# Kernel tuning notes

Measured on AMD Instinct MI355X. Metric: run time of the kernel, lower is better.

Reference implementation:

```python
import jax, jax.numpy as jnp
import numpy as np

# dims
B, T, N, E, ENC, HID, HEADS, D = 64, 128, 2000, 300, 256, 256, 5, 16
IN = ENC + 2 * E          # GRUCell input: assign_emb + program_emb + node_emb
ATT = HID * HEADS         # self-attention context dim (Lin et al. 2017 multi-head)


def setup_inputs() -> dict:
    key = jax.random.key(0)
    ks = jax.random.split(key, 16)
    f = lambda k, shp, s=0.05: jax.random.normal(k, shp, dtype=jnp.float32) * s
    return {
        "program_emb": f(ks[0], (B, ENC), 1.0),
        "h0": f(ks[1], (B, HID), 1.0),                 # xavier-like init h0
        "node_emb": f(ks[2], (N + 1, E)),              # nn.Embedding(num_nodes+1, E)
        "label_emb": f(ks[3], (N + 1, D, E)),          # per-node label embedding experts
        "gru_w_ih": f(ks[4], (3 * HID, IN)),
        "gru_w_hh": f(ks[5], (3 * HID, HID)),
        "gru_b_ih": f(ks[6], (3 * HID,)),
        "gru_b_hh": f(ks[7], (3 * HID,)),
        "attn_ws1": f(ks[8], (HID, HID)),              # SelfAttention ws1 (no bias)
        "attn_ws2": f(ks[9], (HEADS, HID)),            # SelfAttention ws2 (no bias)
        "pred_w": f(ks[10], (N + 1, ATT, D)),          # per-node Linear experts
        "pred_b": f(ks[11], (N + 1, D)),
        "execution_trace": jax.random.randint(ks[12], (B, T), 0, N + 1),
        "node_assignments": jax.random.randint(ks[13], (B, N), 0, D),
        "execution_lengths": jax.random.randint(ks[14], (B,), 1, T + 1),
    }


def _forward(program_emb, h0, node_emb, label_emb, gru_w_ih, gru_w_hh,
             gru_b_ih, gru_b_hh, attn_ws1, attn_ws2, pred_w, pred_b,
             execution_trace, node_assignments):
    # pad assignments with a zero column (PAD node indexes column N)
    na = jnp.concatenate(
        [node_assignments, jnp.zeros((B, 1), node_assignments.dtype)], axis=1)
    rows = jnp.arange(B)
    pos = jnp.arange(T - 1)

    def step(carry, xs):
        h, store = carry
        node_i, node_ip1, i = xs
        # routed label-embedding lookup: expert chosen by node id, row by assignment
        assign_emb = label_emb[node_i, na[rows, node_i]]        # [B,E]
        x = jnp.concatenate([assign_emb, program_emb, node_emb[node_i]], axis=1)
        # torch nn.GRUCell math
        gi = x @ gru_w_ih.T + gru_b_ih
        gh = h @ gru_w_hh.T + gru_b_hh
        ir, iz, inn = jnp.split(gi, 3, axis=1)
        hr, hz, hn = jnp.split(gh, 3, axis=1)
        r = jax.nn.sigmoid(ir + hr)
        z = jax.nn.sigmoid(iz + hz)
        n = jnp.tanh(inn + r * hn)
        h = (1.0 - z) * n + z * h
        # append to growing hidden_store (fixed buffer, step-i slot)
        store = jax.lax.dynamic_update_slice_in_dim(store, h[:, None, :], i, axis=1)
        # structured self-attention over all stored hiddens.
        # NOTE: attn_lengths = max(exec_len, len(store)) >= len(store), so the
        # length mask never hides any stored position; only unwritten slots mask.
        scores = jnp.tanh(store @ attn_ws1.T) @ attn_ws2.T      # [B,T-1,HEADS]
        scores = jnp.where((pos <= i)[None, :, None], scores, -1e9)
        alpha = jax.nn.softmax(scores, axis=1)                  # softmax over time
        ctx = jnp.einsum('bth,btd->bhd', alpha, store).reshape(B, ATT)
        # routed prediction head: expert chosen by next node id (grouped GEMM)
        out = jnp.einsum('bd,bdk->bk', ctx, pred_w[node_ip1]) + pred_b[node_ip1]
        return (h, store), (out, alpha)

    store0 = jnp.zeros((B, T - 1, HID), h0.dtype)
    xs = (execution_trace[:, :-1].T, execution_trace[:, 1:].T, jnp.arange(T - 1))
    (_, _), (outs, alphas) = jax.lax.scan(step, (h0, store0), xs)
    return outs, alphas  # [T-1,B,D], [T-1,B,T-1,HEADS]


def reference(program_emb, h0, node_emb, label_emb, gru_w_ih, gru_w_hh,
              gru_b_ih, gru_b_hh, attn_ws1, attn_ws2, pred_w, pred_b,
              execution_trace, node_assignments, execution_lengths):
    # execution_lengths only enters via max(exec_len, step+1) which never masks;
    # kept for interface fidelity.
    del execution_lengths
    return _forward(program_emb, h0, node_emb, label_emb, gru_w_ih, gru_w_hh,
                    gru_b_ih, gru_b_hh, attn_ws1, attn_ws2, pred_w, pred_b,
                    execution_trace, node_assignments)
```

## Files before the change

kernel.cpp:

```cpp
#include <hip/hip_runtime.h>
#include <hip/hip_bf16.h>
#include <math.h>

#define BB 64
#define TT 128
#define T1 127
#define NNODE 2000
#define EE 300
#define HID 256
#define NHEADS 5
#define DD 16
#define G3 768
#define ATT 1280
#define SCALE_H 28.0f

typedef _Float16 h2_t __attribute__((ext_vector_type(2)));
typedef short short8 __attribute__((ext_vector_type(8)));
typedef float f32x4 __attribute__((ext_vector_type(4)));

__device__ __forceinline__ int dot4(int a, int b, int c) {
#if __has_builtin(__builtin_amdgcn_sdot4)
    return __builtin_amdgcn_sdot4(a, b, c, false);
#else
    int r;
    asm("v_dot4_i32_i8 %0, %1, %2, %3" : "=v"(r) : "v"(a), "v"(b), "v"(c));
    return r;
#endif
}

__device__ __forceinline__ unsigned short f2bf(float f) {
    unsigned u = __float_as_uint(f);
    unsigned r = (u + 0x7FFFu + ((u >> 16) & 1u)) >> 16;
    return (unsigned short)r;
}

__global__ void k_tcvt2(const float* __restrict__ a, unsigned short* __restrict__ da, int Ra, int Ca,
                        const float* __restrict__ b, unsigned short* __restrict__ db, int Rb, int Cb) {
    int idx = blockIdx.x * 256 + threadIdx.x;
    int na = Ra * Ca;
    if (idx < na) {
        int r = idx / Ca, c = idx % Ca;
        da[c * Ra + r] = f2bf(a[idx]);
    } else {
        idx -= na;
        if (idx < Rb * Cb) {
            int r = idx / Cb, c = idx % Cb;
            db[c * Rb + r] = f2bf(b[idx]);
        }
    }
}

__global__ __launch_bounds__(64) void k_quant(const float* __restrict__ w, int* __restrict__ wq,
                                              float* __restrict__ wsc) {
    int row = blockIdx.x;
    int t = threadIdx.x;
    const float* wr = w + (size_t)row * HID;
    float4 v = *(const float4*)(wr + t * 4);
    float m = fmaxf(fmaxf(fabsf(v.x), fabsf(v.y)), fmaxf(fabsf(v.z), fabsf(v.w)));
#pragma unroll
    for (int off = 1; off < 64; off <<= 1) m = fmaxf(m, __shfl_xor(m, off));
    float s = (m > 0.f) ? m * (1.0f / 127.0f) : 1.0f;
    float inv = 1.0f / s;
    int q0 = max(-127, min(127, __float2int_rn(v.x * inv)));
    int q1 = max(-127, min(127, __float2int_rn(v.y * inv)));
    int q2 = max(-127, min(127, __float2int_rn(v.z * inv)));
    int q3 = max(-127, min(127, __float2int_rn(v.w * inv)));
    wq[row * 64 + t] = (q0 & 0xFF) | ((q1 & 0xFF) << 8) | ((q2 & 0xFF) << 16) | ((q3 & 0xFF) << 24);
    if (t == 0) wsc[row] = s;
}

__global__ __launch_bounds__(256) void k_mgemm(
    const float* __restrict__ A, const unsigned short* __restrict__ B16,
    float* __restrict__ out, const float* __restrict__ bias,
    const int* __restrict__ trace, const int* __restrict__ na,
    int mode, int M, int K, int N, int strideA, int ntiles, int brow0, int Bld, int dotanh)
{
    __shared__ short As[64][40];
    __shared__ short Bt[64][40];
    __shared__ int baseLds[64];
    __shared__ int validLds[64];
    int tid = threadIdx.x;
    int bm = blockIdx.x / ntiles, bn = blockIdx.x % ntiles;
    int m0 = bm * 64, n0 = bn * 64;
    if (tid < 64) {
        int m = m0 + tid;
        int valid = (m < M) ? 1 : 0;
        int base = 0;
        if (valid) {
            if (mode == 2) {
                int i = m >> 6, bb = m & 63;
                int node = trace[bb * TT + i];
                int asg = (node < NNODE) ? na[bb * NNODE + node] : 0;
                base = (node * DD + asg) * EE;
            } else {
                base = m * strideA;
            }
        }
        baseLds[tid] = base;
        validLds[tid] = valid;
    }
    __syncthreads();

    int wv = tid >> 6, l = tid & 63;
    int lr = l & 15, lg = l >> 4;
    f32x4 acc[4];
#pragma unroll
    for (int cb = 0; cb < 4; cb++) acc[cb] = (f32x4){0.f, 0.f, 0.f, 0.f};

    int ar = tid >> 2, aq = tid & 3;
    int bk = tid >> 3, bq = tid & 7;
    int nsteps = (K + 31) >> 5;
    for (int it = 0; it < nsteps; it++) {
        int kk = it * 32;
        {
            int base = baseLds[ar], val = validLds[ar];
            short8 t1;
#pragma unroll
            for (int j = 0; j < 8; j++) {
                int kx = kk + aq * 8 + j;
                float v = (val && kx < K) ? A[(size_t)base + kx] : 0.f;
                t1[j] = (short)f2bf(v);
            }
            *(short8*)&As[ar][aq * 8] = t1;
        }
        {
            int kx = kk + bk;
            short8 t2;
            if (kx < K) {
                t2 = *(const short8*)(B16 + (size_t)(brow0 + kx) * Bld + n0 + bq * 8);
            } else {
#pragma unroll
                for (int j = 0; j < 8; j++) t2[j] = 0;
            }
#pragma unroll
            for (int j = 0; j < 8; j++) Bt[bq * 8 + j][bk] = t2[j];
        }
        __syncthreads();
        short8 a = *(const short8*)&As[wv * 16 + lr][lg * 8];
#pragma unroll
        for (int cb = 0; cb < 4; cb++) {
            short8 bfr = *(const short8*)&Bt[cb * 16 + lr][lg * 8];
            acc[cb] = __builtin_amdgcn_mfma_f32_16x16x32_bf16(a, bfr, acc[cb], 0, 0, 0);
        }
        __syncthreads();
    }
#pragma unroll
    for (int cb = 0; cb < 4; cb++) {
        int col = n0 + cb * 16 + lr;
#pragma unroll
        for (int q = 0; q < 4; q++) {
            int row = m0 + wv * 16 + lg * 4 + q;
            if (row < M) {
                float v = acc[cb][q];
                if (bias) v += bias[col];
                if (dotanh) v = tanhf(v);
                out[(size_t)row * N + col] = v;
            }
        }
    }
}

#define LG_PITCH 328
__global__ __launch_bounds__(256) void k_lgemm2(
    const float* __restrict__ A, const unsigned short* __restrict__ B16,
    const float* __restrict__ node_t, const float* __restrict__ prog_t,
    const int* __restrict__ trace, const int* __restrict__ na,
    float* __restrict__ out)
{
    __shared__ short Afull[64][LG_PITCH];
    __shared__ short Bt[64][40];
    __shared__ int nodeLds[64];
    const int tid = threadIdx.x;
    const int ib = blockIdx.x >> 2;
    const int npg = blockIdx.x & 3;

    if (tid < 64) nodeLds[tid] = trace[tid * TT + ib];
    __syncthreads();

#pragma unroll
    for (int g = 0; g < 10; g++) {
        int idx = tid + g * 256;
        int row = idx / 40, c8 = idx % 40;
        int node = nodeLds[row];
        int asg = (node < NNODE) ? na[row * NNODE + node] : 0;
        const float* ap = A + (size_t)(node * DD + asg) * EE;
        short8 t1;
#pragma unroll
        for (int j = 0; j < 8; j++) {
            int kx = c8 * 8 + j;
            float v = (kx < EE) ? ap[kx] : 0.f;
            t1[j] = (short)f2bf(v);
        }
        *(short8*)&Afull[row][c8 * 8] = t1;
    }
    __syncthreads();

    const int wv = tid >> 6, l = tid & 63;
    const int lr = l & 15, lg = l >> 4;
    const int bk = tid >> 3, bq = tid & 7;

    for (int np = npg * 3; np < npg * 3 + 3; np++) {
        int n0 = np * 64;
        f32x4 acc[4];
#pragma unroll
        for (int cb = 0; cb < 4; cb++) acc[cb] = (f32x4){0.f, 0.f, 0.f, 0.f};
#pragma unroll
        for (int ks = 0; ks < 10; ks++) {
            int kx = ks * 32 + bk;
            short8 t2;
            if (kx < EE) {
                t2 = *(const short8*)(B16 + (size_t)kx * G3 + n0 + bq * 8);
            } else {
#pragma unroll
                for (int j = 0; j < 8; j++) t2[j] = 0;
            }
#pragma unroll
            for (int j = 0; j < 8; j++) Bt[bq * 8 + j][bk] = t2[j];
            __syncthreads();
            short8 a = *(const short8*)&Afull[wv * 16 + lr][ks * 32 + lg * 8];
#pragma unroll
            for (int cb = 0; cb < 4; cb++) {
                short8 bfr = *(const short8*)&Bt[cb * 16 + lr][lg * 8];
                acc[cb] = __builtin_amdgcn_mfma_f32_16x16x32_bf16(a, bfr, acc[cb], 0, 0, 0);
            }
            __syncthreads();
        }
#pragma unroll
        for (int cb = 0; cb < 4; cb++) {
            int col = n0 + cb * 16 + lr;
#pragma unroll
            for (int q = 0; q < 4; q++) {
                int rl = wv * 16 + lg * 4 + q;
                int node = nodeLds[rl];
                float v = acc[cb][q] + node_t[(size_t)node * G3 + col] + prog_t[(size_t)rl * G3 + col];
                out[((size_t)ib * 64 + rl) * G3 + col] = v;
            }
        }
    }
}

__global__ __launch_bounds__(512, 2) void rec10_kernel(
    const float* __restrict__ h0, const int* __restrict__ whh8q, const float* __restrict__ wsc,
    const float* __restrict__ bhh, const float* __restrict__ gsum, float* __restrict__ store)
{
    __shared__ float hs32[HID];
    __shared__ int hs8w[HID / 4];
    const int tid = threadIdx.x;
    const int s = tid & 1;
    const int k = tid >> 1;
    const int b = blockIdx.x;

    if (tid < HID) {
        float v = h0[(size_t)b * HID + tid];
        hs32[tid] = v;
        int q = max(-127, min(127, __float2int_rn(v * SCALE_H)));
        ((char*)hs8w)[tid] = (char)q;
    }

    int4 wR[8], wZ[8], wN[8];
    {
        const int4* pr = (const int4*)(whh8q + (size_t)k * 64 + s * 32);
        const int4* pz = (const int4*)(whh8q + (size_t)(HID + k) * 64 + s * 32);
        const int4* pn = (const int4*)(whh8q + (size_t)(2 * HID + k) * 64 + s * 32);
#pragma unroll
        for (int c8 = 0; c8 < 8; c8++) { wR[c8] = pr[c8]; wZ[c8] = pz[c8]; wN[c8] = pn[c8]; }
    }
    const float sR = wsc[k] * (1.0f / SCALE_H);
    const float sZ = wsc[HID + k] * (1.0f / SCALE_H);
    const float sN = wsc[2 * HID + k] * (1.0f / SCALE_H);
    const float bhr = bhh[k], bhz = bhh[HID + k], bhn = bhh[2 * HID + k];
    __syncthreads();

    float gr_c = 0.f, gz_c = 0.f, gn_c = 0.f;
    if (s == 0) {
        const float* lp = gsum + (size_t)b * G3;
        gr_c = lp[k]; gz_c = lp[HID + k]; gn_c = lp[2 * HID + k];
    }

    for (int i = 0; i < T1; i++) {
        float gr_n = 0.f, gz_n = 0.f, gn_n = 0.f;
        if (s == 0 && i + 1 < T1) {
            const float* lp = gsum + ((size_t)(i + 1) * BB + b) * G3;
            gr_n = lp[k]; gz_n = lp[HID + k]; gn_n = lp[2 * HID + k];
        }
        int ar = 0, az = 0, an = 0;
#pragma unroll
        for (int c8 = 0; c8 < 8; c8++) {
            int4 wr = wR[c8], wz = wZ[c8], wn = wN[c8];
            int hv0 = hs8w[s * 32 + c8 * 4 + 0];
            int hv1 = hs8w[s * 32 + c8 * 4 + 1];
            int hv2 = hs8w[s * 32 + c8 * 4 + 2];
            int hv3 = hs8w[s * 32 + c8 * 4 + 3];
            ar = dot4(wr.x, hv0, ar); az = dot4(wz.x, hv0, az); an = dot4(wn.x, hv0, an);
            ar = dot4(wr.y, hv1, ar); az = dot4(wz.y, hv1, az); an = dot4(wn.y, hv1, an);
            ar = dot4(wr.z, hv2, ar); az = dot4(wz.z, hv2, az); an = dot4(wn.z, hv2, an);
            ar = dot4(wr.w, hv3, ar); az = dot4(wz.w, hv3, az); an = dot4(wn.w, hv3, an);
        }
        ar += __shfl_xor(ar, 1); az += __shfl_xor(az, 1); an += __shfl_xor(an, 1);
        __syncthreads();
        if (s == 0) {
            float arf = (float)ar * sR, azf = (float)az * sZ, anf = (float)an * sN;
            float r = 1.f / (1.f + expf(-(gr_c + arf + bhr)));
            float z = 1.f / (1.f + expf(-(gz_c + azf + bhz)));
            float n = tanhf(gn_c + r * (anf + bhn));
            float hold = hs32[k];
            float hnew = (1.f - z) * n + z * hold;
            hs32[k] = hnew;
            store[((size_t)b * T1 + i) * HID + k] = hnew;
            int q = max(-127, min(127, __float2int_rn(hnew * SCALE_H)));
            ((char*)hs8w)[k] = (char)q;
        }
        __syncthreads();
        gr_c = gr_n; gz_c = gz_n; gn_c = gn_n;
    }
}

__global__ void k_scores(const float* __restrict__ U, const float* __restrict__ ws2, float* __restrict__ sbuf) {
    int flat = blockIdx.x * 256 + threadIdx.x;
    if (flat < BB * T1 * NHEADS) {
        int m = flat / NHEADS, h = flat % NHEADS;
        const float* u = U + (size_t)m * HID;
        const float* w = ws2 + h * HID;
        float acc = 0.f;
        for (int c = 0; c < HID; c += 4) {
            float4 u4 = *(const float4*)(u + c);
            float4 w4 = *(const float4*)(w + c);
            acc += u4.x * w4.x + u4.y * w4.y + u4.z * w4.z + u4.w * w4.w;
        }
        sbuf[flat] = acc;
    }
}

__global__ __launch_bounds__(128) void k_softmax_par(const float* __restrict__ sbuf,
                                                     float* __restrict__ ebuf, float* __restrict__ rD) {
    __shared__ float a[128];
    int bh = blockIdx.x;
    int b = bh / NHEADS, h = bh % NHEADS;
    int t = threadIdx.x;
    const float* sp = sbuf + (size_t)b * T1 * NHEADS + h;
    float sv = (t < T1) ? sp[t * NHEADS] : -1e30f;
    a[t] = sv;
    __syncthreads();
#pragma unroll
    for (int off = 64; off >= 1; off >>= 1) {
        if (t < off) a[t] = fmaxf(a[t], a[t + off]);
        __syncthreads();
    }
    float m = a[0];
    __syncthreads();
    float e = (t < T1) ? expf(sv - m) : 0.f;
    a[t] = e;
#pragma unroll
    for (int off = 1; off < 128; off <<= 1) {
        __syncthreads();
        float v = (t >= off) ? a[t - off] : 0.f;
        __syncthreads();
        a[t] += v;
    }
    if (t < T1) {
        ebuf[(b * T1 + t) * NHEADS + h] = e;
        rD[(b * T1 + t) * NHEADS + h] = 1.f / a[t];
    }
}

__global__ void k_alphas(const float* __restrict__ ebuf, const float* __restrict__ rD, float* __restrict__ alph) {
    int flat = blockIdx.x * 256 + threadIdx.x;
    const int TOT = T1 * BB * T1 * NHEADS;
    if (flat < TOT) {
        int i = flat / (BB * T1 * NHEADS);
        int rem = flat % (BB * T1 * NHEADS);
        int b = rem / (T1 * NHEADS);
        int rem2 = rem % (T1 * NHEADS);
        int t = rem2 / NHEADS, h = rem2 % NHEADS;
        float v = 0.f;
        if (t <= i) v = ebuf[(b * T1 + t) * NHEADS + h] * rD[(b * T1 + i) * NHEADS + h];
        alph[flat] = v;
    }
}

__global__ __launch_bounds__(256) void k_ctx(const float* __restrict__ ebuf, const float* __restrict__ rD,
                                             const float* __restrict__ store, unsigned short* __restrict__ ctx16) {
    __shared__ float eL[T1], rL[T1];
    int b = blockIdx.x / NHEADS, h = blockIdx.x % NHEADS;
    int k = threadIdx.x;
    if (k < T1) {
        eL[k] = ebuf[(b * T1 + k) * NHEADS + h];
        rL[k] = rD[(b * T1 + k) * NHEADS + h];
    }
    __syncthreads();
    float acc = 0.f;
#pragma unroll 4
    for (int t = 0; t < T1; t++) {
        acc += eL[t] * store[((size_t)b * T1 + t) * HID + k];
        ctx16[((size_t)t * BB + b) * ATT + h * HID + k] = f2bf(acc * rL[t]);
    }
}

__global__ __launch_bounds__(1024) void k_bucket(const int* __restrict__ trace,
                                                 int* __restrict__ boff, int* __restrict__ items) {
    __shared__ int cnt[NNODE + 1];
    __shared__ int cur[NNODE + 1];
    __shared__ int part[256];
    int t = threadIdx.x;
    for (int x = t; x < NNODE + 1; x += 1024) cnt[x] = 0;
    __syncthreads();
    for (int idx = t; idx < T1 * BB; idx += 1024) {
        int i = idx >> 6, b = idx & 63;
        int node = trace[b * TT + i + 1];
        atomicAdd(&cnt[node], 1);
    }
    __syncthreads();
    int s0 = 0;
    if (t < 256) {
#pragma unroll
        for (int j = 0; j < 8; j++) { int idx = t * 8 + j; if (idx < NNODE + 1) s0 += cnt[idx]; }
        part[t] = s0;
    }
    __syncthreads();
    for (int off = 1; off < 256; off <<= 1) {
        int u = 0;
        if (t < 256 && t >= off) u = part[t - off];
        __syncthreads();
        if (t < 256) part[t] += u;
        __syncthreads();
    }
    if (t < 256) {
        int run = part[t] - s0;
        for (int j = 0; j < 8; j++) {
            int idx = t * 8 + j;
            if (idx < NNODE + 1) { boff[idx] = run; cur[idx] = run; run += cnt[idx]; }
        }
        if (t == 255) boff[NNODE + 1] = part[255];
    }
    __syncthreads();
    for (int idx = t; idx < T1 * BB; idx += 1024) {
        int i = idx >> 6, b = idx & 63;
        int node = trace[b * TT + i + 1];
        int pos = atomicAdd(&cur[node], 1);
        items[pos] = idx;
    }
}

__global__ __launch_bounds__(256) void k_pred2(
    const unsigned short* __restrict__ ctx16, const float* __restrict__ pw, const float* __restrict__ pb,
    const int* __restrict__ boff, const int* __restrict__ items, float* __restrict__ outs)
{
    __shared__ float cl[8][ATT];
    __shared__ float red[16][16][8];
    int e = blockIdx.x;
    int start = boff[e], end = boff[e + 1];
    if (start == end) return;
    int tid = threadIdx.x;
    int d = tid & 15, ks = tid >> 4;
    const float* w = pw + (size_t)e * ATT * DD;
    float biasv = pb[e * DD + d];
    for (int c0 = start; c0 < end; c0 += 8) {
        int cn = min(8, end - c0);
        for (int j = 0; j < cn; j++) {
            int item = items[c0 + j];
            const unsigned short* cp = ctx16 + (size_t)item * ATT;
            for (int x = tid; x < ATT; x += 256)
                cl[j][x] = __uint_as_float((unsigned)cp[x] << 16);
        }
        __syncthreads();
        float acc[8];
#pragma unroll
        for (int j = 0; j < 8; j++) acc[j] = 0.f;
        for (int kx = ks * 80; kx < ks * 80 + 80; kx++) {
            float wv = w[kx * DD + d];
#pragma unroll
            for (int j = 0; j < 8; j++) acc[j] += cl[j][kx] * wv;
        }
#pragma unroll
        for (int j = 0; j < 8; j++) red[ks][d][j] = acc[j];
        __syncthreads();
#pragma unroll
        for (int st = 8; st >= 1; st >>= 1) {
            if (ks < st) {
#pragma unroll
                for (int j = 0; j < 8; j++) red[ks][d][j] += red[ks + st][d][j];
            }
            __syncthreads();
        }
        if (ks == 0) {
            for (int j = 0; j < cn; j++) {
                int item = items[c0 + j];
                outs[(size_t)item * DD + d] = red[0][d][j] + biasv;
            }
        }
        __syncthreads();
    }
}

extern "C" void kernel_launch(void* const* d_in, const int* in_sizes, int n_in,
                              void* d_out, int out_size, void* d_ws, size_t ws_size,
                              hipStream_t stream) {
    const float* program_emb = (const float*)d_in[0];
    const float* h0       = (const float*)d_in[1];
    const float* node_emb = (const float*)d_in[2];
    const float* label_emb= (const float*)d_in[3];
    const float* w_ih     = (const float*)d_in[4];
    const float* w_hh     = (const float*)d_in[5];
    const float* b_ih     = (const float*)d_in[6];
    const float* b_hh     = (const float*)d_in[7];
    const float* ws1      = (const float*)d_in[8];
    const float* ws2      = (const float*)d_in[9];
    const float* pred_w   = (const float*)d_in[10];
    const float* pred_b   = (const float*)d_in[11];
    const int*   trace    = (const int*)d_in[12];
    const int*   na       = (const int*)d_in[13];

    float*          ws      = (float*)d_ws;
    float*          store   = ws + 0;
    unsigned short* wihT16  = (unsigned short*)(ws + 2080768);
    unsigned short* ws1T16  = (unsigned short*)(ws + 2409472);
    float*          prog_t  = ws + 2803712;
    float*          node_t  = ws + 2852864;
    float*          sbuf    = ws + 4389632;
    float*          ebuf    = ws + 4430272;
    float*          rD      = ws + 4470912;
    float*          label_p = ws + 4511568;
    float*          Ubuf    = ws + 10753872;
    int*            whh8q   = (int*)(ws + 12834640);
    float*          wsc     = ws + 12883792;
    unsigned short* ctx16   = (unsigned short*)(ws + 4511568);
    int*            cnt_    = (int*)(ws + 2080768);
    int*            boff    = cnt_ + 4096;
    int*            items   = boff + 2048;

    float* outs = (float*)d_out;
    float* alph = outs + T1 * BB * DD;

    k_tcvt2<<<2824, 256, 0, stream>>>(w_ih, wihT16, G3, 856, ws1, ws1T16, HID, HID);
    k_quant<<<G3, 64, 0, stream>>>(w_hh, whh8q, wsc);
    k_mgemm<<<12,   256, 0, stream>>>(program_emb, wihT16, prog_t, b_ih,   nullptr, nullptr, 0, 64,   256, G3,  256, 12, 300, G3, 0);
    k_mgemm<<<384,  256, 0, stream>>>(node_emb,    wihT16, node_t, nullptr, nullptr, nullptr, 0, 2001, 300, G3,  300, 12, 556, G3, 0);
    k_lgemm2<<<508, 256, 0, stream>>>(label_emb, wihT16, node_t, prog_t, trace, na, label_p);

    rec10_kernel<<<64, 512, 0, stream>>>(h0, whh8q, wsc, b_hh, label_p, store);

    k_mgemm<<<508, 256, 0, stream>>>(store, ws1T16, Ubuf, nullptr, nullptr, nullptr, 0, 8128, 256, HID, 256, 4, 0, HID, 1);
    k_scores<<<159, 256, 0, stream>>>(Ubuf, ws2, sbuf);
    k_softmax_par<<<BB * NHEADS, 128, 0, stream>>>(sbuf, ebuf, rD);
    k_alphas<<<20162, 256, 0, stream>>>(ebuf, rD, alph);
    k_ctx<<<320, 256, 0, stream>>>(ebuf, rD, store, ctx16);

    k_bucket<<<1, 1024, 0, stream>>>(trace, boff, items);
    k_pred2<<<NNODE + 1, 256, 0, stream>>>(ctx16, pred_w, pred_b, boff, items, outs);
}
```

Before: 372.6 us.

## Fuse ws1 GEMM with tanh and score projection; widen GRU recurrence split

Two changes. The recurrent GRU kernel now uses 4 threads per hidden unit instead of 2 (1024 threads per block), which halves each thread's int8 dot-product chain per step at the cost of an extra shuffle reduction. The separate ws1 GEMM and score kernels are merged into one MFMA kernel. It keeps tanh(U) in LDS as bf16 and computes the 5 head scores directly, which removes the U buffer round trip to global memory and one launch. The fused kernel runs only 127 blocks, and rounding U to bf16 adds some precision loss.

```diff
diff --git a/kernel.cpp b/kernel.cpp
--- a/kernel.cpp
+++ b/kernel.cpp
@@ -32,6 +32,10 @@
     unsigned u = __float_as_uint(f);
     unsigned r = (u + 0x7FFFu + ((u >> 16) & 1u)) >> 16;
     return (unsigned short)r;
+}
+
+__device__ __forceinline__ float bf2f(unsigned short u) {
+    return __uint_as_float((unsigned)u << 16);
 }
 
 __global__ void k_tcvt2(const float* __restrict__ a, unsigned short* __restrict__ da, int Ra, int Ca,
@@ -239,15 +243,15 @@
     }
 }
 
-__global__ __launch_bounds__(512, 2) void rec10_kernel(
+__global__ __launch_bounds__(1024) void rec11_kernel(
     const float* __restrict__ h0, const int* __restrict__ whh8q, const float* __restrict__ wsc,
     const float* __restrict__ bhh, const float* __restrict__ gsum, float* __restrict__ store)
 {
     __shared__ float hs32[HID];
     __shared__ int hs8w[HID / 4];
     const int tid = threadIdx.x;
-    const int s = tid & 1;
-    const int k = tid >> 1;
+    const int s = tid & 3;
+    const int k = tid >> 2;
     const int b = blockIdx.x;
 
     if (tid < HID) {
@@ -257,13 +261,13 @@
         ((char*)hs8w)[tid] = (char)q;
     }
 
-    int4 wR[8], wZ[8], wN[8];
+    int4 wR[4], wZ[4], wN[4];
     {
-        const int4* pr = (const int4*)(whh8q + (size_t)k * 64 + s * 32);
-        const int4* pz = (const int4*)(whh8q + (size_t)(HID + k) * 64 + s * 32);
-        const int4* pn = (const int4*)(whh8q + (size_t)(2 * HID + k) * 64 + s * 32);
-#pragma unroll
-        for (int c8 = 0; c8 < 8; c8++) { wR[c8] = pr[c8]; wZ[c8] = pz[c8]; wN[c8] = pn[c8]; }
+        const int4* pr = (const int4*)(whh8q + (size_t)k * 64 + s * 16);
+        const int4* pz = (const int4*)(whh8q + (size_t)(HID + k) * 64 + s * 16);
+        const int4* pn = (const int4*)(whh8q + (size_t)(2 * HID + k) * 64 + s * 16);
+#pragma unroll
+        for (int c8 = 0; c8 < 4; c8++) { wR[c8] = pr[c8]; wZ[c8] = pz[c8]; wN[c8] = pn[c8]; }
     }
     const float sR = wsc[k] * (1.0f / SCALE_H);
     const float sZ = wsc[HID + k] * (1.0f / SCALE_H);
@@ -285,18 +289,19 @@
         }
         int ar = 0, az = 0, an = 0;
 #pragma unroll
-        for (int c8 = 0; c8 < 8; c8++) {
+        for (int c8 = 0; c8 < 4; c8++) {
             int4 wr = wR[c8], wz = wZ[c8], wn = wN[c8];
-            int hv0 = hs8w[s * 32 + c8 * 4 + 0];
-            int hv1 = hs8w[s * 32 + c8 * 4 + 1];
-            int hv2 = hs8w[s * 32 + c8 * 4 + 2];
-            int hv3 = hs8w[s * 32 + c8 * 4 + 3];
+            int hv0 = hs8w[s * 16 + c8 * 4 + 0];
+            int hv1 = hs8w[s * 16 + c8 * 4 + 1];
+            int hv2 = hs8w[s * 16 + c8 * 4 + 2];
+            int hv3 = hs8w[s * 16 + c8 * 4 + 3];
             ar = dot4(wr.x, hv0, ar); az = dot4(wz.x, hv0, az); an = dot4(wn.x, hv0, an);
             ar = dot4(wr.y, hv1, ar); az = dot4(wz.y, hv1, az); an = dot4(wn.y, hv1, an);
             ar = dot4(wr.z, hv2, ar); az = dot4(wz.z, hv2, az); an = dot4(wn.z, hv2, an);
             ar = dot4(wr.w, hv3, ar); az = dot4(wz.w, hv3, az); an = dot4(wn.w, hv3, an);
         }
         ar += __shfl_xor(ar, 1); az += __shfl_xor(az, 1); an += __shfl_xor(an, 1);
+        ar += __shfl_xor(ar, 2); az += __shfl_xor(az, 2); an += __shfl_xor(an, 2);
         __syncthreads();
         if (s == 0) {
             float arf = (float)ar * sR, azf = (float)az * sZ, anf = (float)an * sN;
@@ -315,19 +320,77 @@
     }
 }
 
-__global__ void k_scores(const float* __restrict__ U, const float* __restrict__ ws2, float* __restrict__ sbuf) {
-    int flat = blockIdx.x * 256 + threadIdx.x;
-    if (flat < BB * T1 * NHEADS) {
-        int m = flat / NHEADS, h = flat % NHEADS;
-        const float* u = U + (size_t)m * HID;
-        const float* w = ws2 + h * HID;
+#define US_PITCH 264
+__global__ __launch_bounds__(256) void k_uscore(
+    const float* __restrict__ store, const unsigned short* __restrict__ ws1T16,
+    const float* __restrict__ ws2, float* __restrict__ sbuf)
+{
+    __shared__ short As[64][US_PITCH];
+    __shared__ short Ub[64][US_PITCH];
+    __shared__ short Bt[64][40];
+    const int tid = threadIdx.x;
+    const int m0 = blockIdx.x * 64;
+
+#pragma unroll
+    for (int g = 0; g < 8; g++) {
+        int idx = tid + g * 256;
+        int row = idx >> 5, c8 = idx & 31;
+        const float* ap = store + (size_t)(m0 + row) * HID + c8 * 8;
+        short8 t1;
+#pragma unroll
+        for (int j = 0; j < 8; j++) t1[j] = (short)f2bf(ap[j]);
+        *(short8*)&As[row][c8 * 8] = t1;
+    }
+    __syncthreads();
+
+    const int wv = tid >> 6, l = tid & 63;
+    const int lr = l & 15, lg = l >> 4;
+    const int bk = tid >> 3, bq = tid & 7;
+
+    for (int np = 0; np < 4; np++) {
+        int n0 = np * 64;
+        f32x4 acc[4];
+#pragma unroll
+        for (int cb = 0; cb < 4; cb++) acc[cb] = (f32x4){0.f, 0.f, 0.f, 0.f};
+#pragma unroll
+        for (int ks = 0; ks < 8; ks++) {
+            int kx = ks * 32 + bk;
+            short8 t2 = *(const short8*)(ws1T16 + (size_t)kx * HID + n0 + bq * 8);
+#pragma unroll
+            for (int j = 0; j < 8; j++) Bt[bq * 8 + j][bk] = t2[j];
+            __syncthreads();
+            short8 a = *(const short8*)&As[wv * 16 + lr][ks * 32 + lg * 8];
+#pragma unroll
+            for (int cb = 0; cb < 4; cb++) {
+                short8 bfr = *(const short8*)&Bt[cb * 16 + lr][lg * 8];
+                acc[cb] = __builtin_amdgcn_mfma_f32_16x16x32_bf16(a, bfr, acc[cb], 0, 0, 0);
+            }
+            __syncthreads();
+        }
+#pragma unroll
+        for (int cb = 0; cb < 4; cb++) {
+            int col = n0 + cb * 16 + lr;
+#pragma unroll
+            for (int q = 0; q < 4; q++) {
+                int row = wv * 16 + lg * 4 + q;
+                Ub[row][col] = (short)f2bf(tanhf(acc[cb][q]));
+            }
+        }
+    }
+    __syncthreads();
+
+    for (int d = tid; d < 64 * NHEADS; d += 256) {
+        int row = d / NHEADS, h = d % NHEADS;
+        const float* w2 = ws2 + h * HID;
         float acc = 0.f;
-        for (int c = 0; c < HID; c += 4) {
-            float4 u4 = *(const float4*)(u + c);
-            float4 w4 = *(const float4*)(w + c);
-            acc += u4.x * w4.x + u4.y * w4.y + u4.z * w4.z + u4.w * w4.w;
-        }
-        sbuf[flat] = acc;
+#pragma unroll 4
+        for (int c = 0; c < HID; c += 8) {
+            short8 u8 = *(const short8*)&Ub[row][c];
+#pragma unroll
+            for (int j = 0; j < 8; j++)
+                acc += bf2f((unsigned short)u8[j]) * w2[c + j];
+        }
+        sbuf[(size_t)(m0 + row) * NHEADS + h] = acc;
     }
 }
 
@@ -460,7 +523,7 @@
             int item = items[c0 + j];
             const unsigned short* cp = ctx16 + (size_t)item * ATT;
             for (int x = tid; x < ATT; x += 256)
-                cl[j][x] = __uint_as_float((unsigned)cp[x] << 16);
+                cl[j][x] = bf2f(cp[x]);
         }
         __syncthreads();
         float acc[8];
@@ -520,7 +583,6 @@
     float*          ebuf    = ws + 4430272;
     float*          rD      = ws + 4470912;
     float*          label_p = ws + 4511568;
-    float*          Ubuf    = ws + 10753872;
     int*            whh8q   = (int*)(ws + 12834640);
     float*          wsc     = ws + 12883792;
     unsigned short* ctx16   = (unsigned short*)(ws + 4511568);
@@ -537,10 +599,9 @@
     k_mgemm<<<384,  256, 0, stream>>>(node_emb,    wihT16, node_t, nullptr, nullptr, nullptr, 0, 2001, 300, G3,  300, 12, 556, G3, 0);
     k_lgemm2<<<508, 256, 0, stream>>>(label_emb, wihT16, node_t, prog_t, trace, na, label_p);
 
-    rec10_kernel<<<64, 512, 0, stream>>>(h0, whh8q, wsc, b_hh, label_p, store);
-
-    k_mgemm<<<508, 256, 0, stream>>>(store, ws1T16, Ubuf, nullptr, nullptr, nullptr, 0, 8128, 256, HID, 256, 4, 0, HID, 1);
-    k_scores<<<159, 256, 0, stream>>>(Ubuf, ws2, sbuf);
+    rec11_kernel<<<64, 1024, 0, stream>>>(h0, whh8q, wsc, b_hh, label_p, store);
+
+    k_uscore<<<127, 256, 0, stream>>>(store, ws1T16, ws2, sbuf);
     k_softmax_par<<<BB * NHEADS, 128, 0, stream>>>(sbuf, ebuf, rD);
     k_alphas<<<20162, 256, 0, stream>>>(ebuf, rD, alph);
     k_ctx<<<320, 256, 0, stream>>>(ebuf, rD, store, ctx16);
```

After: 403.3 us. +8.2%, slower.
